# Performance work log

Hardware: AMD Instinct MI355X
Metric: run time of the kernel (lower is better)

Reference implementation:

```python
import math
import jax, jax.numpy as jnp
import numpy as np

TWO_PI = 2.0 * math.pi
EPS = 1e-6

F_DELTA, F_THETA, F_GAMMA = 2.0, 6.0, 40.0  # hard-coded band frequencies (Hz)
K_COUPLING = 2.0
N_STEPS = 10
DT = 0.01


def setup_inputs() -> dict:
    key = jax.random.key(0)
    ks = jax.random.split(key, 4)
    B, D = 32768, 2048
    nd, nt, ng = 32, 128, 512

    def xavier(k, fan_out, fan_in, gain=0.5):
        lim = gain * math.sqrt(6.0 / (fan_in + fan_out))
        return jax.random.uniform(k, (fan_out, fan_in), jnp.float32, -lim, lim)

    return {
        "x": jax.random.normal(ks[0], (B, D), jnp.float32),
        "W_delta": xavier(ks[1], nd, D),
        "W_theta": xavier(ks[2], nt, D),
        "W_gamma": xavier(ks[3], ng, D),
        "pac_depth_dt": jnp.float32(0.3),
        "pac_depth_tg": jnp.float32(0.3),
    }


def _mean_field(phase):
    # Kuramoto order parameter components, per batch row. phase: (B, n)
    C = jnp.mean(jnp.cos(phase), axis=-1, keepdims=True)
    S = jnp.mean(jnp.sin(phase), axis=-1, keepdims=True)
    return C, S


def _dynamics(dp, da, tp, ta, gp, ga, pac_dt, pac_tg):
    """Batched 3-band Kuramoto integration with cross-frequency PAC.

    Phases evolve under mean-field Kuramoto coupling within each band;
    the slow band's mean phase amplitude-modulates the next-faster band
    (delta->theta via pac_dt, theta->gamma via pac_tg). Euler, N_STEPS x DT.
    """
    def step(carry, _):
        dp, da, tp, ta, gp, ga = carry
        Cd, Sd = _mean_field(dp)
        Ct, St = _mean_field(tp)
        Cg, Sg = _mean_field(gp)
        # K * r * sin(psi - phi) == K * (S*cos(phi) - C*sin(phi))
        dp_n = (dp + DT * (TWO_PI * F_DELTA + K_COUPLING * (Sd * jnp.cos(dp) - Cd * jnp.sin(dp)))) % TWO_PI
        tp_n = (tp + DT * (TWO_PI * F_THETA + K_COUPLING * (St * jnp.cos(tp) - Ct * jnp.sin(tp)))) % TWO_PI
        gp_n = (gp + DT * (TWO_PI * F_GAMMA + K_COUPLING * (Sg * jnp.cos(gp) - Cg * jnp.sin(gp)))) % TWO_PI
        rd = jnp.sqrt(Cd * Cd + Sd * Sd) + EPS
        rt = jnp.sqrt(Ct * Ct + St * St) + EPS
        ta_n = jnp.maximum(ta * (1.0 + DT * pac_dt * (Cd / rd)), EPS)
        ga_n = jnp.maximum(ga * (1.0 + DT * pac_tg * (Ct / rt)), EPS)
        return (dp_n, da, tp_n, ta_n, gp_n, ga_n), None

    (dp, da, tp, ta, gp, ga), _ = jax.lax.scan(step, (dp, da, tp, ta, gp, ga), None, length=N_STEPS)
    return dp, da, tp, ta, gp, ga


def reference(x, W_delta, W_theta, W_gamma, pac_depth_dt, pac_depth_tg):
    # Three small dense projections define initial phases and amplitudes.
    zd = x @ W_delta.T  # (B, n_delta)
    zt = x @ W_theta.T  # (B, n_theta)
    zg = x @ W_gamma.T  # (B, n_gamma)
    da, ta, ga = (jnp.maximum(jnp.abs(z), EPS) for z in (zd, zt, zg))
    dp, tp, gp = (z % TWO_PI for z in (zd, zt, zg))
    # pac depths are detached in the torch module (.item()) before dynamics
    pac_dt = jax.lax.stop_gradient(jnp.clip(pac_depth_dt, 0.0, 1.0))
    pac_tg = jax.lax.stop_gradient(jnp.clip(pac_depth_tg, 0.0, 1.0))
    _, da, _, ta, _, ga = _dynamics(dp, da, tp, ta, gp, ga, pac_dt, pac_tg)
    return jnp.concatenate([da, ta, ga], axis=-1)  # (B, n_total)
```

## Files before the change

kernel.cpp:

```cpp
#include <hip/hip_runtime.h>
#include <stdint.h>

#define TWO_PI_F 6.28318530717958647692f
#define INV_2PI_F 0.15915494309189535f
#define EPSF 1e-6f
#define DTF 0.01f
#define KCOUP 2.0f
#define CPL (DTF * KCOUP * INV_2PI_F)

#define BM 128
#define BN 96
#define KITERS 32
#define NTILES 7
#define GTHREADS 256
#define B_TILE_BYTES (BN * 128)
#define A_TILE_BYTES (BM * 256)
#define WCHUNK (672 * 128)
#define W_IMG_BYTES ((size_t)KITERS * WCHUNK)
#define WS_NEED W_IMG_BYTES

typedef __attribute__((ext_vector_type(8)))  __bf16         bf16x8;
typedef __attribute__((ext_vector_type(8)))  unsigned short ushort8v;
typedef __attribute__((ext_vector_type(16))) float          f32x16;

__device__ __forceinline__ unsigned short f2bf(float f) {
  unsigned u = __builtin_bit_cast(unsigned, f);
  u = (u + 0x7FFFu + ((u >> 16) & 1u)) >> 16;
  return (unsigned short)u;
}

__device__ __forceinline__ unsigned cvtpk(float lo, float hi) {
  unsigned r;
  asm("v_cvt_pk_bf16_f32 %0, %1, %2" : "=v"(r) : "v"(lo), "v"(hi));
  return r;
}

__global__ void prep_w(const float* __restrict__ Wd, const float* __restrict__ Wt,
                       const float* __restrict__ Wg, char* __restrict__ wbB) {
  int id = blockIdx.x * 256 + threadIdx.x;
  if (id >= 672 * 64) return;
  int col = id >> 6;
  int rem = id & 63, t = rem >> 1, h = rem & 1;
  const float* src = (col < 32)  ? Wd + (size_t)col * 2048
                   : (col < 160) ? Wt + (size_t)(col - 32) * 2048
                                 : Wg + (size_t)(col - 160) * 2048;
  src += t * 64 + h * 32;
  char* dst = wbB + ((size_t)t * 672 + col) * 128;
  #pragma unroll
  for (int s4 = 0; s4 < 4; s4++) {
    float4 a = ((const float4*)src)[s4 * 2];
    float4 b = ((const float4*)src)[s4 * 2 + 1];
    ushort8v v;
    v[0] = f2bf(a.x); v[1] = f2bf(a.y); v[2] = f2bf(a.z); v[3] = f2bf(a.w);
    v[4] = f2bf(b.x); v[5] = f2bf(b.y); v[6] = f2bf(b.z); v[7] = f2bf(b.w);
    int slot = (h * 4 + s4) ^ (col & 7);
    *(ushort8v*)(dst + slot * 16) = v;
  }
}

__launch_bounds__(GTHREADS, 3)
__global__ void gemm(const float* __restrict__ x, const char* __restrict__ wbB,
                     float* __restrict__ z) {
  __shared__ __align__(16) char smem[B_TILE_BYTES + A_TILE_BYTES];
  char* Bs = smem;
  char* As = smem + B_TILE_BYTES;

  const int tid = threadIdx.x;
  const int wid = tid >> 6, lane = tid & 63;

  const int bid = blockIdx.x;
  const int xcd = bid & 7, j = bid >> 3;
  const int panel = xcd * 32 + j / NTILES;
  const int n = j % NTILES;
  const size_t row0 = (size_t)panel * BM;

  f32x16 acc[3];
  #pragma unroll
  for (int f = 0; f < 3; f++)
    #pragma unroll
    for (int jj = 0; jj < 16; jj++) acc[f][jj] = 0.f;

  const int arow_s = tid >> 4;
  const int aslot_log = (tid & 15) ^ arow_s;
  const float* asrc0 = x + (row0 + arow_s) * 2048 + aslot_log * 4;

  const int arf = wid * 32 + (lane & 31);
  const float* afbase = (const float*)(As + arf * 256);
  const int arfx = arf & 15;

  for (int t = 0; t < KITERS; t++) {
    __syncthreads();
    {
      const char* bsrc = wbB + (size_t)t * WCHUNK + n * B_TILE_BYTES;
      #pragma unroll
      for (int rnd = 0; rnd < 3; rnd++) {
        int off = rnd * 4096 + tid * 16;
        __builtin_amdgcn_global_load_lds(
            (const __attribute__((address_space(1))) void*)(bsrc + off),
            (__attribute__((address_space(3))) void*)(Bs + off), 16, 0, 0);
      }
      const float* asrc = asrc0 + t * 64;
      #pragma unroll
      for (int rnd = 0; rnd < 8; rnd++) {
        __builtin_amdgcn_global_load_lds(
            (const __attribute__((address_space(1))) void*)(asrc + (size_t)rnd * 16 * 2048),
            (__attribute__((address_space(3))) void*)(As + rnd * 4096 + tid * 16), 16, 0, 0);
      }
    }
    __syncthreads();
    #pragma unroll
    for (int s4 = 0; s4 < 4; s4++) {
      int sl = s4 * 2 + (lane >> 5);
      int ls = s4 * 4 + (lane >> 5) * 2;
      int p0 = ls ^ arfx;
      int p1 = p0 ^ 1;
      float4 lo = *(const float4*)(afbase + p0 * 4);
      float4 hi = *(const float4*)(afbase + p1 * 4);
      unsigned d0 = cvtpk(lo.x, lo.y), d1 = cvtpk(lo.z, lo.w);
      unsigned d2 = cvtpk(hi.x, hi.y), d3 = cvtpk(hi.z, hi.w);
      uint4 u = {d0, d1, d2, d3};
      bf16x8 af = __builtin_bit_cast(bf16x8, u);
      #pragma unroll
      for (int fn = 0; fn < 3; fn++) {
        int c = fn * 32 + (lane & 31);
        bf16x8 bfr = __builtin_bit_cast(bf16x8,
            *(const ushort8v*)(Bs + c * 128 + ((sl ^ (c & 7)) << 4)));
        acc[fn] = __builtin_amdgcn_mfma_f32_32x32x16_bf16(af, bfr, acc[fn], 0, 0, 0);
      }
    }
  }

  #pragma unroll
  for (int fn = 0; fn < 3; fn++) {
    int col = n * 96 + fn * 32 + (lane & 31);
    #pragma unroll
    for (int reg = 0; reg < 16; reg++) {
      int row = wid * 32 + (reg & 3) + ((reg >> 2) << 3) + ((lane >> 5) << 2);
      z[(row0 + row) * 672 + col] = acc[fn][reg];
    }
  }
}

__device__ __forceinline__ float wave_sum(float v) {
  v += __builtin_bit_cast(float, __builtin_amdgcn_update_dpp(
         0, __builtin_bit_cast(int, v), 0xB1, 0xF, 0xF, true));
  v += __builtin_bit_cast(float, __builtin_amdgcn_update_dpp(
         0, __builtin_bit_cast(int, v), 0x4E, 0xF, 0xF, true));
  v += __builtin_bit_cast(float, __builtin_amdgcn_update_dpp(
         0, __builtin_bit_cast(int, v), 0x141, 0xF, 0xF, true));
  v += __builtin_bit_cast(float, __builtin_amdgcn_update_dpp(
         0, __builtin_bit_cast(int, v), 0x140, 0xF, 0xF, true));
  v += __builtin_bit_cast(float, __builtin_amdgcn_ds_swizzle(
         __builtin_bit_cast(int, v), 0x401F));
  v += __shfl_xor(v, 32);
  return v;
}

#define ZSTR 164
#define DROWS 32
__launch_bounds__(256, 6)
__global__ void dyn_scale(float* __restrict__ z,
                          const float* __restrict__ pdt_p,
                          const float* __restrict__ ptg_p) {
  __shared__ float zdt[DROWS * ZSTR];
  __shared__ float Fbuf[2 * DROWS];
  const int tid = threadIdx.x;
  const int wid = tid >> 6, lane = tid & 63;
  const size_t row0 = (size_t)blockIdx.x * DROWS;

  for (int i = tid; i < DROWS * 40; i += 256) {
    int row = i / 40, c4 = i - row * 40;
    float4 v = *(const float4*)(z + (row0 + row) * 672 + c4 * 4);
    *(float4*)(&zdt[row * ZSTR + c4 * 4]) = v;
  }
  __syncthreads();

  const float pdt = fminf(fmaxf(pdt_p[0], 0.f), 1.f);
  const float ptg = fminf(fmaxf(ptg_p[0], 0.f), 1.f);

  for (int rr = 0; rr < 8; rr++) {
    int row = wid * 8 + rr;
    float pd  = ((lane < 32) ? zdt[row * ZSTR + lane] : 0.f) * INV_2PI_F;
    float pt0 = zdt[row * ZSTR + 32 + lane] * INV_2PI_F;
    float pt1 = zdt[row * ZSTR + 96 + lane] * INV_2PI_F;
    float Ft = 1.f, Fg = 1.f;
    for (int s = 0; s < 10; s++) {
      float qd = pd - floorf(pd), q0 = pt0 - floorf(pt0), q1 = pt1 - floorf(pt1);
      float sd, cd, s0, c0, s1, c1;
      asm("v_sin_f32 %0, %1" : "=v"(sd) : "v"(qd));
      asm("v_cos_f32 %0, %1" : "=v"(cd) : "v"(qd));
      asm("v_sin_f32 %0, %1" : "=v"(s0) : "v"(q0));
      asm("v_cos_f32 %0, %1" : "=v"(c0) : "v"(q0));
      asm("v_sin_f32 %0, %1" : "=v"(s1) : "v"(q1));
      asm("v_cos_f32 %0, %1" : "=v"(c1) : "v"(q1));
      float Cd = wave_sum((lane < 32) ? cd : 0.f) * (1.f / 32.f);
      float Sd = wave_sum((lane < 32) ? sd : 0.f) * (1.f / 32.f);
      float Ct = wave_sum(c0 + c1) * (1.f / 128.f);
      float St = wave_sum(s0 + s1) * (1.f / 128.f);
      pd  += DTF * 2.f + CPL * (Sd * cd - Cd * sd);
      pt0 += DTF * 6.f + CPL * (St * c0 - Ct * s0);
      pt1 += DTF * 6.f + CPL * (St * c1 - Ct * s1);
      float rdm = sqrtf(Cd * Cd + Sd * Sd) + EPSF;
      float rtm = sqrtf(Ct * Ct + St * St) + EPSF;
      Ft *= (1.f + DTF * pdt * (Cd / rdm));
      Fg *= (1.f + DTF * ptg * (Ct / rtm));
    }
    if (lane == 0) { Fbuf[row] = Ft; Fbuf[DROWS + row] = Fg; }
  }
  __syncthreads();

  for (int i = tid; i < DROWS * 168; i += 256) {
    int row = i / 168, c4 = i - row * 168;
    float4* p = (float4*)(z + (row0 + row) * 672 + c4 * 4);
    float4 v = (c4 < 40) ? *(const float4*)(&zdt[row * ZSTR + c4 * 4]) : *p;
    float f = (c4 < 8) ? 1.f : (c4 < 40 ? Fbuf[row] : Fbuf[DROWS + row]);
    v.x = fmaxf(fmaxf(fabsf(v.x), EPSF) * f, EPSF);
    v.y = fmaxf(fmaxf(fabsf(v.y), EPSF) * f, EPSF);
    v.z = fmaxf(fmaxf(fabsf(v.z), EPSF) * f, EPSF);
    v.w = fmaxf(fmaxf(fabsf(v.w), EPSF) * f, EPSF);
    *p = v;
  }
}

extern "C" void kernel_launch(void* const* d_in, const int* in_sizes, int n_in,
                              void* d_out, int out_size, void* d_ws, size_t ws_size,
                              hipStream_t stream) {
  const float* x   = (const float*)d_in[0];
  const float* Wd  = (const float*)d_in[1];
  const float* Wt  = (const float*)d_in[2];
  const float* Wg  = (const float*)d_in[3];
  const float* pdt = (const float*)d_in[4];
  const float* ptg = (const float*)d_in[5];
  float* outp = (float*)d_out;
  char* wbB = (char*)d_ws;

  if (ws_size < WS_NEED) return;

  const int Brows = in_sizes[0] / 2048;
  prep_w<<<(672 * 64 + 255) / 256, 256, 0, stream>>>(Wd, Wt, Wg, wbB);
  gemm<<<(Brows / BM) * NTILES, GTHREADS, 0, stream>>>(x, wbB, outp);
  dyn_scale<<<Brows / DROWS, 256, 0, stream>>>(outp, pdt, ptg);
}
```

Before: 265.7 us.

## Load W fragments directly to registers with double-buffered prefetch instead of LDS

Repacks the bf16 weight image into an MFMA-fragment-ordered layout so each lane loads its B operand straight from global memory into registers, removing the B tile from LDS. The main loop is restructured into a software pipeline: next iteration's B fragments are prefetched into a second register set, and the A tile for the next step is issued after compute, with explicit vmcnt waits and barriers. The aim is to overlap global loads with MFMA work and cut LDS traffic, at the cost of more VGPRs (24 extra bf16x8 registers), which may hurt occupancy. The manual waitcnt counting is fragile.

New measurement: 340.1 us. 1.28x slower.

```diff
diff --git a/kernel.cpp b/kernel.cpp
--- a/kernel.cpp
+++ b/kernel.cpp
@@ -13,10 +13,8 @@
 #define KITERS 32
 #define NTILES 7
 #define GTHREADS 256
-#define B_TILE_BYTES (BN * 128)
 #define A_TILE_BYTES (BM * 256)
-#define WCHUNK (672 * 128)
-#define W_IMG_BYTES ((size_t)KITERS * WCHUNK)
+#define W_IMG_BYTES ((size_t)32 * 4 * 21 * 64 * 16)
 #define WS_NEED W_IMG_BYTES
 
 typedef __attribute__((ext_vector_type(8)))  __bf16         bf16x8;
@@ -44,26 +42,24 @@
   const float* src = (col < 32)  ? Wd + (size_t)col * 2048
                    : (col < 160) ? Wt + (size_t)(col - 32) * 2048
                                  : Wg + (size_t)(col - 160) * 2048;
-  src += t * 64 + h * 32;
-  char* dst = wbB + ((size_t)t * 672 + col) * 128;
+  const int ct = col >> 5, lane = h * 32 + (col & 31);
   #pragma unroll
   for (int s4 = 0; s4 < 4; s4++) {
-    float4 a = ((const float4*)src)[s4 * 2];
-    float4 b = ((const float4*)src)[s4 * 2 + 1];
+    const float* kp = src + t * 64 + s4 * 16 + h * 8;
+    float4 a = ((const float4*)kp)[0];
+    float4 b = ((const float4*)kp)[1];
     ushort8v v;
     v[0] = f2bf(a.x); v[1] = f2bf(a.y); v[2] = f2bf(a.z); v[3] = f2bf(a.w);
     v[4] = f2bf(b.x); v[5] = f2bf(b.y); v[6] = f2bf(b.z); v[7] = f2bf(b.w);
-    int slot = (h * 4 + s4) ^ (col & 7);
-    *(ushort8v*)(dst + slot * 16) = v;
+    char* dst = wbB + ((((size_t)t * 4 + s4) * 21 + ct) * 64 + lane) * 16;
+    *(ushort8v*)dst = v;
   }
 }
 
 __launch_bounds__(GTHREADS, 3)
 __global__ void gemm(const float* __restrict__ x, const char* __restrict__ wbB,
                      float* __restrict__ z) {
-  __shared__ __align__(16) char smem[B_TILE_BYTES + A_TILE_BYTES];
-  char* Bs = smem;
-  char* As = smem + B_TILE_BYTES;
+  __shared__ __align__(16) char As[A_TILE_BYTES];
 
   const int tid = threadIdx.x;
   const int wid = tid >> 6, lane = tid & 63;
@@ -88,47 +84,70 @@
   const float* afbase = (const float*)(As + arf * 256);
   const int arfx = arf & 15;
 
-  for (int t = 0; t < KITERS; t++) {
-    __syncthreads();
-    {
-      const char* bsrc = wbB + (size_t)t * WCHUNK + n * B_TILE_BYTES;
-      #pragma unroll
-      for (int rnd = 0; rnd < 3; rnd++) {
-        int off = rnd * 4096 + tid * 16;
-        __builtin_amdgcn_global_load_lds(
-            (const __attribute__((address_space(1))) void*)(bsrc + off),
-            (__attribute__((address_space(3))) void*)(Bs + off), 16, 0, 0);
-      }
-      const float* asrc = asrc0 + t * 64;
-      #pragma unroll
-      for (int rnd = 0; rnd < 8; rnd++) {
-        __builtin_amdgcn_global_load_lds(
-            (const __attribute__((address_space(1))) void*)(asrc + (size_t)rnd * 16 * 2048),
-            (__attribute__((address_space(3))) void*)(As + rnd * 4096 + tid * 16), 16, 0, 0);
-      }
-    }
-    __syncthreads();
-    #pragma unroll
-    for (int s4 = 0; s4 < 4; s4++) {
-      int sl = s4 * 2 + (lane >> 5);
-      int ls = s4 * 4 + (lane >> 5) * 2;
-      int p0 = ls ^ arfx;
-      int p1 = p0 ^ 1;
-      float4 lo = *(const float4*)(afbase + p0 * 4);
-      float4 hi = *(const float4*)(afbase + p1 * 4);
-      unsigned d0 = cvtpk(lo.x, lo.y), d1 = cvtpk(lo.z, lo.w);
-      unsigned d2 = cvtpk(hi.x, hi.y), d3 = cvtpk(hi.z, hi.w);
-      uint4 u = {d0, d1, d2, d3};
-      bf16x8 af = __builtin_bit_cast(bf16x8, u);
-      #pragma unroll
-      for (int fn = 0; fn < 3; fn++) {
-        int c = fn * 32 + (lane & 31);
-        bf16x8 bfr = __builtin_bit_cast(bf16x8,
-            *(const ushort8v*)(Bs + c * 128 + ((sl ^ (c & 7)) << 4)));
-        acc[fn] = __builtin_amdgcn_mfma_f32_32x32x16_bf16(af, bfr, acc[fn], 0, 0, 0);
-      }
-    }
-  }
+  const char* bbase = wbB + (size_t)(n * 3) * 1024 + (size_t)lane * 16;
+
+#define STAGE_A(t)                                                            \
+  { const float* asrc = asrc0 + (t) * 64;                                     \
+    _Pragma("unroll")                                                         \
+    for (int rnd = 0; rnd < 8; rnd++) {                                       \
+      __builtin_amdgcn_global_load_lds(                                       \
+          (const __attribute__((address_space(1))) void*)(asrc + (size_t)rnd * 16 * 2048), \
+          (__attribute__((address_space(3))) void*)(As + rnd * 4096 + tid * 16), 16, 0, 0); } }
+
+#define LOADB(arr, t)                                                         \
+  { _Pragma("unroll")                                                         \
+    for (int s4 = 0; s4 < 4; s4++)                                            \
+      _Pragma("unroll")                                                       \
+      for (int fn = 0; fn < 3; fn++)                                          \
+        arr[s4][fn] = *(const ushort8v*)(bbase +                              \
+            ((size_t)((t) * 4 + s4) * 21 + fn) * 1024); }
+
+#define COMPUTE(BC)                                                           \
+  { _Pragma("unroll")                                                         \
+    for (int s4 = 0; s4 < 4; s4++) {                                          \
+      int ls = s4 * 4 + (lane >> 5) * 2;                                      \
+      int p0 = ls ^ arfx;                                                     \
+      int p1 = p0 ^ 1;                                                        \
+      float4 lo = *(const float4*)(afbase + p0 * 4);                          \
+      float4 hi = *(const float4*)(afbase + p1 * 4);                          \
+      unsigned d0 = cvtpk(lo.x, lo.y), d1 = cvtpk(lo.z, lo.w);                \
+      unsigned d2 = cvtpk(hi.x, hi.y), d3 = cvtpk(hi.z, hi.w);                \
+      uint4 u = {d0, d1, d2, d3};                                             \
+      bf16x8 af = __builtin_bit_cast(bf16x8, u);                              \
+      _Pragma("unroll")                                                       \
+      for (int fn = 0; fn < 3; fn++) {                                        \
+        bf16x8 bfr = __builtin_bit_cast(bf16x8, BC[s4][fn]);                  \
+        acc[fn] = __builtin_amdgcn_mfma_f32_32x32x16_bf16(af, bfr, acc[fn], 0, 0, 0); } } }
+
+#define BODY(t, BC, BNx)                                                      \
+  {                                                                           \
+    if ((t) + 1 < KITERS) {                                                   \
+      LOADB(BNx, (t) + 1);                                                    \
+      asm volatile("s_waitcnt vmcnt(12)" ::: "memory");                       \
+    } else {                                                                  \
+      asm volatile("s_waitcnt vmcnt(0)" ::: "memory");                        \
+    }                                                                         \
+    __builtin_amdgcn_s_barrier();                                             \
+    __builtin_amdgcn_sched_barrier(0);                                        \
+    COMPUTE(BC);                                                              \
+    __builtin_amdgcn_sched_barrier(0);                                        \
+    __builtin_amdgcn_s_barrier();                                             \
+    if ((t) + 1 < KITERS) { STAGE_A((t) + 1); }                               \
+  }
+
+  ushort8v BA[4][3], BB[4][3];
+
+  LOADB(BA, 0);
+  STAGE_A(0);
+
+  for (int tt = 0; tt < KITERS; tt += 2) {
+    BODY(tt,     BA, BB);
+    BODY(tt + 1, BB, BA);
+  }
+#undef STAGE_A
+#undef LOADB
+#undef COMPUTE
+#undef BODY
 
   #pragma unroll
   for (int fn = 0; fn < 3; fn++) {
```
